# Performance work log

Hardware: AMD Instinct MI355X
Metric: run time of the kernel (lower is better)

Reference implementation:

```python
import jax, jax.numpy as jnp
import numpy as np

B, S, H, NH = 2, 2048, 1024, 16
HD = H // NH  # head_dim = 64
ROPE_BASE = 10000.0


def _rope(x):
    # x: [B, NH, S, HD]; LLaMA-style half-split rotary embedding
    s, d = x.shape[2], x.shape[3]
    inv_freq = 1.0 / (ROPE_BASE ** (jnp.arange(0, d, 2, dtype=jnp.float32) / d))  # [d/2]
    ang = jnp.arange(s, dtype=jnp.float32)[:, None] * inv_freq[None, :]            # [S, d/2]
    cos, sin = jnp.cos(ang), jnp.sin(ang)
    x1, x2 = x[..., : d // 2], x[..., d // 2:]
    return jnp.concatenate([x1 * cos - x2 * sin, x1 * sin + x2 * cos], axis=-1)


def setup_inputs() -> dict:
    key = jax.random.key(0)
    ks = jax.random.split(key, 9)
    hidden_states = jax.random.normal(ks[0], (B, S, H), dtype=jnp.float32)
    # causal mask: True = attend
    causal = jnp.tril(jnp.ones((S, S), dtype=bool))
    attention_mask = jnp.broadcast_to(causal[None, None, :, :], (B, 1, S, S))
    std = 0.02
    wq = jax.random.normal(ks[1], (H, NH * HD), dtype=jnp.float32) * std
    wk = jax.random.normal(ks[2], (H, NH * HD), dtype=jnp.float32) * std
    wv = jax.random.normal(ks[3], (H, NH * HD), dtype=jnp.float32) * std
    wo = jax.random.normal(ks[4], (NH * HD, H), dtype=jnp.float32) * std
    bq = jnp.zeros((NH * HD,), dtype=jnp.float32)
    bk = jnp.zeros((NH * HD,), dtype=jnp.float32)
    bv = jnp.zeros((NH * HD,), dtype=jnp.float32)
    bo = jnp.zeros((H,), dtype=jnp.float32)
    return {"hidden_states": hidden_states, "attention_mask": attention_mask,
            "wq": wq, "bq": bq, "wk": wk, "bk": bk, "wv": wv, "bv": bv,
            "wo": wo, "bo": bo}


def _split_heads(x):
    b, s, _ = x.shape
    return jnp.transpose(x.reshape(b, s, NH, HD), (0, 2, 1, 3))


def reference(hidden_states, attention_mask, wq, bq, wk, bk, wv, bv, wo, bo):
    q = _split_heads(hidden_states @ wq + bq)  # [B,NH,S,HD]
    k = _split_heads(hidden_states @ wk + bk)
    v = _split_heads(hidden_states @ wv + bv)
    q = _rope(q)
    k = _rope(k)
    scores = jnp.einsum('bhqd,bhkd->bhqk', q, k) / jnp.sqrt(jnp.float32(HD))
    scores = jnp.where(attention_mask, scores, jnp.float32(-1e9))
    weights = jax.nn.softmax(scores, axis=-1)
    attn = jnp.einsum('bhqk,bhkv->bhqv', weights, v)  # [B,NH,S,HD]
    attn = jnp.transpose(attn, (0, 2, 1, 3)).reshape(hidden_states.shape[0], attn.shape[2], H)
    return attn @ wo + bo
```

## Files before the change

### kernel.cpp

```cpp
#include <hip/hip_runtime.h>
#include <math.h>

typedef short bf16x8 __attribute__((ext_vector_type(8)));
typedef float f32x4  __attribute__((ext_vector_type(4)));

__device__ __forceinline__ unsigned short f2bf(float f) {
    union { float f; unsigned u; } v; v.f = f;
    unsigned r = v.u + 0x7FFFu + ((v.u >> 16) & 1u);
    return (unsigned short)(r >> 16);
}

#define GLDS16(gp, lp) __builtin_amdgcn_global_load_lds( \
    (const __attribute__((address_space(1))) void*)(gp), \
    (__attribute__((address_space(3))) void*)(lp), 16, 0, 0)


__global__ __launch_bounds__(256)
void prep(const float* __restrict__ X, unsigned short* __restrict__ Xb,
          const float* __restrict__ w0, const float* __restrict__ w1,
          const float* __restrict__ w2, const float* __restrict__ w3,
          unsigned short* o0, unsigned short* o1,
          unsigned short* o2, unsigned short* o3)
{
    const int z = blockIdx.z;
    if (z >= 4) {
        const int lb = (z - 4) * 256 + blockIdx.y * 16 + blockIdx.x;
        const size_t t = (size_t)lb * 256 + threadIdx.x;
        const float4 a = *(const float4*)(X + t * 8);
        const float4 b = *(const float4*)(X + t * 8 + 4);
        unsigned short u[8] = { f2bf(a.x), f2bf(a.y), f2bf(a.z), f2bf(a.w),
                                f2bf(b.x), f2bf(b.y), f2bf(b.z), f2bf(b.w) };
        *(int4*)(Xb + t * 8) = *(int4*)u;
        return;
    }
    const float* W; unsigned short* O;
    switch (z) {
        case 0: W = w0; O = o0; break;
        case 1: W = w1; O = o1; break;
        case 2: W = w2; O = o2; break;
        default: W = w3; O = o3; break;
    }
    __shared__ float T[64][65];
    const int tid = threadIdx.x;
    const int n0 = blockIdx.x * 64, k0 = blockIdx.y * 64;
    #pragma unroll
    for (int i = 0; i < 4; i++) {
        const int k = (tid >> 4) + i * 16, n4 = (tid & 15) * 4;
        const float4 v = *(const float4*)(W + (size_t)(k0 + k) * 1024 + n0 + n4);
        T[k][n4] = v.x; T[k][n4+1] = v.y; T[k][n4+2] = v.z; T[k][n4+3] = v.w;
    }
    __syncthreads();
    if (z == 3) {
        #pragma unroll
        for (int i = 0; i < 4; i++) {
            const int n = (tid >> 4) + i * 16, k4 = (tid & 15) * 4;
            unsigned short u[4];
            #pragma unroll
            for (int j = 0; j < 4; j++) {
                const int q = k4 + j;
                const int p = (q & 3) * 16 + (q >> 2);
                const int d = (p & 3) * 16 + (p >> 2);
                u[j] = f2bf(T[d][n]);
            }
            *(int2*)(O + (size_t)(n0 + n) * 1024 + k0 + k4) = *(int2*)u;
        }
    } else {
        #pragma unroll
        for (int i = 0; i < 4; i++) {
            const int n = (tid >> 4) + i * 16, k4 = (tid & 15) * 4;
            unsigned short u[4] = { f2bf(T[k4][n]), f2bf(T[k4+1][n]),
                                    f2bf(T[k4+2][n]), f2bf(T[k4+3][n]) };
            *(int2*)(O + (size_t)(n0 + n) * 1024 + k0 + k4) = *(int2*)u;
        }
    }
}

__global__ __launch_bounds__(256)
void transpose_v(const unsigned short* __restrict__ Vb, unsigned short* __restrict__ Vtb)
{
    __shared__ unsigned short T[64][72];
    const int tid = threadIdx.x, bh = blockIdx.y, s0 = blockIdx.x * 64;
    const size_t base = (size_t)bh * 2048 * 64;
    #pragma unroll
    for (int i = 0; i < 2; i++) {
        const int s = (tid >> 3) + i * 32, d8 = (tid & 7) * 8;
        *(int4*)&T[s][d8] = *(const int4*)(Vb + base + (size_t)(s0 + s) * 64 + d8);
    }
    __syncthreads();
    #pragma unroll
    for (int i = 0; i < 2; i++) {
        const int d = (tid >> 3) + i * 32, s8 = (tid & 7) * 8;
        unsigned short u[8];
        #pragma unroll
        for (int j = 0; j < 8; j++) u[j] = T[s8 + j][d];
        *(int4*)(Vtb + base + (size_t)d * 2048 + s0 + s8) = *(int4*)u;
    }
}

__global__ __launch_bounds__(256)
void qkv_gemm(const unsigned short* __restrict__ Xb,
              const unsigned short* __restrict__ Wtq, const unsigned short* __restrict__ Wtk,
              const unsigned short* __restrict__ Wtv,
              const float* __restrict__ bq, const float* __restrict__ bk,
              const float* __restrict__ bv,
              unsigned short* __restrict__ Qb, unsigned short* __restrict__ Kb,
              unsigned short* __restrict__ Vb)
{
    const unsigned short* Wt; const float* bias; unsigned short* Out;
    const int z = blockIdx.z;
    if (z == 0)      { Wt = Wtq; bias = bq; Out = Qb; }
    else if (z == 1) { Wt = Wtk; bias = bk; Out = Kb; }
    else             { Wt = Wtv; bias = bv; Out = Vb; }

    __shared__ unsigned short As[128 * 32];
    __shared__ unsigned short Bs[128 * 32];
    const int tid = threadIdx.x, lane = tid & 63, w = tid >> 6;
    const int quad = lane >> 4, c = lane & 15;
    const int wr = w >> 1, wc = w & 1;
    const int m0 = blockIdx.x * 128, n0 = blockIdx.y * 128;
    const int srow = lane >> 2, scol = (lane & 3) * 8;

    f32x4 acc[4][4];
    #pragma unroll
    for (int i = 0; i < 4; i++)
        #pragma unroll
        for (int j = 0; j < 4; j++) acc[i][j] = (f32x4){0.f, 0.f, 0.f, 0.f};

    for (int k0 = 0; k0 < 1024; k0 += 32) {
        #pragma unroll
        for (int j = 0; j < 2; j++) {
            const int r = w * 32 + j * 16;
            GLDS16(Xb + (size_t)(m0 + r + srow) * 1024 + k0 + scol, &As[r * 32]);
            GLDS16(Wt + (size_t)(n0 + r + srow) * 1024 + k0 + scol, &Bs[r * 32]);
        }
        __syncthreads();
        bf16x8 af[4], bf[4];
        #pragma unroll
        for (int rt = 0; rt < 4; rt++)
            af[rt] = *(const bf16x8*)&As[(wr * 64 + rt * 16 + c) * 32 + quad * 8];
        #pragma unroll
        for (int nt = 0; nt < 4; nt++)
            bf[nt] = *(const bf16x8*)&Bs[(wc * 64 + nt * 16 + c) * 32 + quad * 8];
        #pragma unroll
        for (int rt = 0; rt < 4; rt++)
            #pragma unroll
            for (int nt = 0; nt < 4; nt++)
                acc[rt][nt] = __builtin_amdgcn_mfma_f32_16x16x32_bf16(af[rt], bf[nt], acc[rt][nt], 0, 0, 0);
        __syncthreads();
    }

    const int h = (n0 + wc * 64) >> 6;
    const bool rope = (z < 2);
    const float kLn = 9.210340371976184f / 32.0f;
    const float TWO_PI_INV = 0.15915494309189535f;
    const float rv0 = expf(-(float)c * kLn) * TWO_PI_INV;
    const float rv1 = expf(-(float)(c + 16) * kLn) * TWO_PI_INV;
    float bv4[4];
    #pragma unroll
    for (int nt = 0; nt < 4; nt++) bv4[nt] = bias[n0 + wc * 64 + nt * 16 + c];

    #pragma unroll
    for (int rt = 0; rt < 4; rt++) {
        #pragma unroll
        for (int reg = 0; reg < 4; reg++) {
            const int m = m0 + wr * 64 + rt * 16 + quad * 4 + reg;
            const int b = m >> 11, s = m & 2047;
            float x0 = acc[rt][0][reg] + bv4[0];
            float x1 = acc[rt][1][reg] + bv4[1];
            float x2 = acc[rt][2][reg] + bv4[2];
            float x3 = acc[rt][3][reg] + bv4[3];
            float y0 = x0, y1 = x1, y2 = x2, y3 = x3;
            if (rope) {
                float r0 = (float)s * rv0;  r0 -= floorf(r0);
                float r1 = (float)s * rv1;  r1 -= floorf(r1);
                const float sn0 = __builtin_amdgcn_sinf(r0);
                const float cs0 = __builtin_amdgcn_cosf(r0);
                const float sn1 = __builtin_amdgcn_sinf(r1);
                const float cs1 = __builtin_amdgcn_cosf(r1);
                y0 = x0 * cs0 - x2 * sn0;  y2 = x0 * sn0 + x2 * cs0;
                y1 = x1 * cs1 - x3 * sn1;  y3 = x1 * sn1 + x3 * cs1;
            }
            unsigned short u[4] = { f2bf(y0), f2bf(y1), f2bf(y2), f2bf(y3) };
            unsigned short* dst = Out + ((size_t)(b * 16 + h) * 2048 + s) * 64;
            *(int2*)(dst + c * 4) = *(int2*)u;
        }
    }
}

__global__ __launch_bounds__(256)
void out_gemm(const unsigned short* __restrict__ Ab, const unsigned short* __restrict__ Wto,
              const float* __restrict__ bo, float* __restrict__ Out)
{
    __shared__ unsigned short As[128 * 32];
    __shared__ unsigned short Bs[128 * 32];
    const int tid = threadIdx.x, lane = tid & 63, w = tid >> 6;
    const int quad = lane >> 4, c = lane & 15;
    const int wr = w >> 1, wc = w & 1;
    const int m0 = blockIdx.x * 128, n0 = blockIdx.y * 128;
    const int srow = lane >> 2, scol = (lane & 3) * 8;

    f32x4 acc[4][4];
    #pragma unroll
    for (int i = 0; i < 4; i++)
        #pragma unroll
        for (int j = 0; j < 4; j++) acc[i][j] = (f32x4){0.f, 0.f, 0.f, 0.f};

    for (int k0 = 0; k0 < 1024; k0 += 32) {
        #pragma unroll
        for (int j = 0; j < 2; j++) {
            const int r = w * 32 + j * 16;
            GLDS16(Ab  + (size_t)(m0 + r + srow) * 1024 + k0 + scol, &As[r * 32]);
            GLDS16(Wto + (size_t)(n0 + r + srow) * 1024 + k0 + scol, &Bs[r * 32]);
        }
        __syncthreads();
        bf16x8 af[4], bf[4];
        #pragma unroll
        for (int rt = 0; rt < 4; rt++)
            af[rt] = *(const bf16x8*)&As[(wr * 64 + rt * 16 + c) * 32 + quad * 8];
        #pragma unroll
        for (int nt = 0; nt < 4; nt++)
            bf[nt] = *(const bf16x8*)&Bs[(wc * 64 + nt * 16 + c) * 32 + quad * 8];
        #pragma unroll
        for (int rt = 0; rt < 4; rt++)
            #pragma unroll
            for (int nt = 0; nt < 4; nt++)
                acc[rt][nt] = __builtin_amdgcn_mfma_f32_16x16x32_bf16(af[rt], bf[nt], acc[rt][nt], 0, 0, 0);
        __syncthreads();
    }
    #pragma unroll
    for (int rt = 0; rt < 4; rt++) {
        #pragma unroll
        for (int reg = 0; reg < 4; reg++) {
            const int m = m0 + wr * 64 + rt * 16 + quad * 4 + reg;
            #pragma unroll
            for (int nt = 0; nt < 4; nt++) {
                const int n = n0 + wc * 64 + nt * 16 + c;
                Out[(size_t)m * 1024 + n] = acc[rt][nt][reg] + bo[n];
            }
        }
    }
}

__global__ __launch_bounds__(256)
void attn_part(const unsigned short* __restrict__ Qb, const unsigned short* __restrict__ Kb,
               const unsigned short* __restrict__ Vtb, unsigned short* __restrict__ Ab,
               float* __restrict__ Opart, float* __restrict__ Lpart)
{
    __shared__ unsigned short Ks[64 * 72];
    __shared__ unsigned short Vs[65 * 72];
    __shared__ unsigned short Ps[4 * 16 * 72];

    const int tid = threadIdx.x, w = tid >> 6, lane = tid & 63;
    const int quad = lane >> 4, c = lane & 15;
    const int bh = blockIdx.y;
    const int x = (blockIdx.x < 32) ? (int)blockIdx.x + 16 : (int)blockIdx.x - 32;
    int i, start, len;
    if (x < 32) { i = x + 1;  start = 0;  len = (i < 16) ? i : 16; }
    else        { i = x - 15; start = 16; len = i - 16; }
    const int q0 = (i - 1) * 64;
    const bool complete = (start == 0) && (len == i);
    const size_t base = (size_t)bh * 2048 * 64;

    if (tid < 64) Vs[64 * 72 + tid] = 0x3F80;

    const int qbase = q0 + w * 16;
    const int qrow  = qbase + c;
    const size_t qoff = base + (size_t)qrow * 64;
    const bf16x8 qf0 = *(const bf16x8*)(Qb + qoff + quad * 8);
    const bf16x8 qf1 = *(const bf16x8*)(Qb + qoff + 32 + quad * 8);

    f32x4 O[4], Osum;
    Osum = (f32x4){0.f, 0.f, 0.f, 0.f};
    #pragma unroll
    for (int nt = 0; nt < 4; nt++) O[nt] = (f32x4){0.f, 0.f, 0.f, 0.f};

    const int r0s = tid >> 3, r1s = r0s + 32, c8 = (tid & 7) * 8;

    int k0 = start * 64;
    int4 kreg0 = *(const int4*)(Kb  + base + (size_t)(k0 + r0s) * 64 + c8);
    int4 kreg1 = *(const int4*)(Kb  + base + (size_t)(k0 + r1s) * 64 + c8);
    int4 vreg0 = *(const int4*)(Vtb + base + (size_t)r0s * 2048 + k0 + c8);
    int4 vreg1 = *(const int4*)(Vtb + base + (size_t)r1s * 2048 + k0 + c8);

    unsigned short* Pw = Ps + w * 16 * 72;

    for (int t = 0; t < len; t++, k0 += 64) {
        *(int4*)&Ks[(size_t)r0s * 72 + c8] = kreg0;
        *(int4*)&Ks[(size_t)r1s * 72 + c8] = kreg1;
        *(int4*)&Vs[(size_t)r0s * 72 + c8] = vreg0;
        *(int4*)&Vs[(size_t)r1s * 72 + c8] = vreg1;
        __syncthreads();

        if (t + 1 < len) {
            const int kn = k0 + 64;
            kreg0 = *(const int4*)(Kb  + base + (size_t)(kn + r0s) * 64 + c8);
            kreg1 = *(const int4*)(Kb  + base + (size_t)(kn + r1s) * 64 + c8);
            vreg0 = *(const int4*)(Vtb + base + (size_t)r0s * 2048 + kn + c8);
            vreg1 = *(const int4*)(Vtb + base + (size_t)r1s * 2048 + kn + c8);
        }

        const bool need_mask = (k0 + 63) > qbase;

        #pragma unroll
        for (int nt = 0; nt < 4; nt++) {
            const bf16x8 kf0 = *(const bf16x8*)&Ks[(nt * 16 + c) * 72 + quad * 8];
            const bf16x8 kf1 = *(const bf16x8*)&Ks[(nt * 16 + c) * 72 + 32 + quad * 8];
            f32x4 s4 = (f32x4){0.f, 0.f, 0.f, 0.f};
            s4 = __builtin_amdgcn_mfma_f32_16x16x32_bf16(kf0, qf0, s4, 0, 0, 0);
            s4 = __builtin_amdgcn_mfma_f32_16x16x32_bf16(kf1, qf1, s4, 0, 0, 0);
            const int keyb = k0 + nt * 16 + quad * 4;
            unsigned short u[4];
            #pragma unroll
            for (int reg = 0; reg < 4; reg++) {
                float p = __expf(s4[reg] * 0.125f);
                if (need_mask && (keyb + reg > qrow)) p = 0.f;
                u[reg] = f2bf(p);
            }
            *(int2*)&Pw[c * 72 + nt * 16 + quad * 4] = *(int2*)u;
        }

        const bf16x8 pa0 = *(const bf16x8*)&Pw[c * 72 + quad * 8];
        const bf16x8 pa1 = *(const bf16x8*)&Pw[c * 72 + 32 + quad * 8];
        #pragma unroll
        for (int nt = 0; nt < 4; nt++) {
            const bf16x8 vb0 = *(const bf16x8*)&Vs[(nt * 16 + c) * 72 + quad * 8];
            const bf16x8 vb1 = *(const bf16x8*)&Vs[(nt * 16 + c) * 72 + 32 + quad * 8];
            O[nt] = __builtin_amdgcn_mfma_f32_16x16x32_bf16(pa0, vb0, O[nt], 0, 0, 0);
            O[nt] = __builtin_amdgcn_mfma_f32_16x16x32_bf16(pa1, vb1, O[nt], 0, 0, 0);
        }
        const bf16x8 on0 = *(const bf16x8*)&Vs[64 * 72 + quad * 8];
        const bf16x8 on1 = *(const bf16x8*)&Vs[64 * 72 + 32 + quad * 8];
        Osum = __builtin_amdgcn_mfma_f32_16x16x32_bf16(pa0, on0, Osum, 0, 0, 0);
        Osum = __builtin_amdgcn_mfma_f32_16x16x32_bf16(pa1, on1, Osum, 0, 0, 0);
        __syncthreads();
    }

    if (complete) {
        const int b = bh >> 4, h = bh & 15;
        #pragma unroll
        for (int reg = 0; reg < 4; reg++) {
            const float inv = 1.0f / Osum[reg];
            const int q = qbase + quad * 4 + reg;
            unsigned short u[4];
            #pragma unroll
            for (int nt = 0; nt < 4; nt++) u[nt] = f2bf(O[nt][reg] * inv);
            unsigned short* dst = Ab + ((size_t)(b * 2048 + q)) * 1024 + h * 64;
            *(int2*)(dst + c * 4) = *(int2*)u;
        }
    } else {
        const int pslot = (i - 17) * 2 + (start ? 1 : 0);
        float* Op = Opart + ((size_t)bh * 32 + pslot) * 4096;
        float* Lp = Lpart + ((size_t)bh * 32 + pslot) * 64;
        #pragma unroll
        for (int reg = 0; reg < 4; reg++) {
            const int row = w * 16 + quad * 4 + reg;
            float4 o4 = make_float4(O[0][reg], O[1][reg], O[2][reg], O[3][reg]);
            *(float4*)(Op + (size_t)row * 64 + c * 4) = o4;
            if (c == 0) Lp[row] = Osum[reg];
        }
    }
}

__global__ __launch_bounds__(256)
void attn_combine(const float* __restrict__ Opart, const float* __restrict__ Lpart,
                  unsigned short* __restrict__ Ab)
{
    const int tid = threadIdx.x;
    const int j = blockIdx.x, bh = blockIdx.y;
    const int q0 = (j + 16) * 64;
    const size_t s0 = ((size_t)bh * 32 + j * 2) * 4096;
    const size_t l0 = ((size_t)bh * 32 + j * 2) * 64;

    __shared__ float linv[64];
    if (tid < 64) linv[tid] = 1.0f / (Lpart[l0 + tid] + Lpart[l0 + 64 + tid]);
    __syncthreads();

    const int row = tid >> 2, col0 = (tid & 3) * 16;
    const float inv = linv[row];
    const int b = bh >> 4, h = bh & 15;
    const int q = q0 + row;
    unsigned short* dst = Ab + ((size_t)(b * 2048 + q)) * 1024 + h * 64 + col0;
    #pragma unroll
    for (int c4 = 0; c4 < 16; c4 += 4) {
        const float4 a  = *(const float4*)(Opart + s0 + (size_t)row * 64 + col0 + c4);
        const float4 bb = *(const float4*)(Opart + s0 + 4096 + (size_t)row * 64 + col0 + c4);
        dst[c4 + 0] = f2bf((a.x + bb.x) * inv);
        dst[c4 + 1] = f2bf((a.y + bb.y) * inv);
        dst[c4 + 2] = f2bf((a.z + bb.z) * inv);
        dst[c4 + 3] = f2bf((a.w + bb.w) * inv);
    }
}

extern "C" void kernel_launch(void* const* d_in, const int* in_sizes, int n_in,
                              void* d_out, int out_size, void* d_ws, size_t ws_size,
                              hipStream_t stream)
{
    const float* X  = (const float*)d_in[0];
    const float* wq = (const float*)d_in[2];
    const float* bq = (const float*)d_in[3];
    const float* wk = (const float*)d_in[4];
    const float* bk = (const float*)d_in[5];
    const float* wv = (const float*)d_in[6];
    const float* bv = (const float*)d_in[7];
    const float* wo = (const float*)d_in[8];
    const float* bo = (const float*)d_in[9];

    unsigned short* ws = (unsigned short*)d_ws;
    const size_t M1 = 1024 * 1024;
    unsigned short* Xb  = ws;
    unsigned short* Wtq = Xb  + 4 * M1;
    unsigned short* Wtk = Wtq + M1;
    unsigned short* Wtv = Wtk + M1;
    unsigned short* Wto = Wtv + M1;
    unsigned short* Qb  = Wto + M1;
    unsigned short* Kb  = Qb  + 4 * M1;
    unsigned short* Vb  = Kb  + 4 * M1;
    unsigned short* Vtb = Vb  + 4 * M1;
    unsigned short* Ab  = Vtb + 4 * M1;
    float* Opart = (float*)(Ab + 4 * M1);
    float* Lpart = Opart + (size_t)32 * 32 * 4096;

    prep        <<<dim3(16, 16, 12), 256, 0, stream>>>(X, Xb, wq, wk, wv, wo,
                                                       Wtq, Wtk, Wtv, Wto);
    qkv_gemm    <<<dim3(32, 8, 3), 256, 0, stream>>>(Xb, Wtq, Wtk, Wtv, bq, bk, bv, Qb, Kb, Vb);
    transpose_v <<<dim3(32, 32), 256, 0, stream>>>(Vb, Vtb);
    attn_part   <<<dim3(48, 32), 256, 0, stream>>>(Qb, Kb, Vtb, Ab, Opart, Lpart);
    attn_combine<<<dim3(16, 32), 256, 0, stream>>>(Opart, Lpart, Ab);
    out_gemm    <<<dim3(32, 8), 256, 0, stream>>>(Ab, Wto, bo, (float*)d_out);
}
```

Before: 228.5 us.

## Fuse V transpose into QKV GEMM epilogue and double GEMM K-step

The V projection now writes its output directly in the transposed [bh, d, s] layout from the QKV GEMM epilogue, which removes the separate transpose_v kernel launch and one read-write pass over V. Both GEMMs also process 64 K-elements per iteration using two LDS sub-tiles, which halves the number of barrier pairs per tile. The cost is doubled shared memory per block, which may reduce occupancy, and the transposed V stores are narrow 8-byte writes strided by 2048 elements.

```diff
diff --git a/kernel.cpp b/kernel.cpp
--- a/kernel.cpp
+++ b/kernel.cpp
@@ -76,44 +76,22 @@
 }
 
 __global__ __launch_bounds__(256)
-void transpose_v(const unsigned short* __restrict__ Vb, unsigned short* __restrict__ Vtb)
-{
-    __shared__ unsigned short T[64][72];
-    const int tid = threadIdx.x, bh = blockIdx.y, s0 = blockIdx.x * 64;
-    const size_t base = (size_t)bh * 2048 * 64;
-    #pragma unroll
-    for (int i = 0; i < 2; i++) {
-        const int s = (tid >> 3) + i * 32, d8 = (tid & 7) * 8;
-        *(int4*)&T[s][d8] = *(const int4*)(Vb + base + (size_t)(s0 + s) * 64 + d8);
-    }
-    __syncthreads();
-    #pragma unroll
-    for (int i = 0; i < 2; i++) {
-        const int d = (tid >> 3) + i * 32, s8 = (tid & 7) * 8;
-        unsigned short u[8];
-        #pragma unroll
-        for (int j = 0; j < 8; j++) u[j] = T[s8 + j][d];
-        *(int4*)(Vtb + base + (size_t)d * 2048 + s0 + s8) = *(int4*)u;
-    }
-}
-
-__global__ __launch_bounds__(256)
 void qkv_gemm(const unsigned short* __restrict__ Xb,
               const unsigned short* __restrict__ Wtq, const unsigned short* __restrict__ Wtk,
               const unsigned short* __restrict__ Wtv,
               const float* __restrict__ bq, const float* __restrict__ bk,
               const float* __restrict__ bv,
               unsigned short* __restrict__ Qb, unsigned short* __restrict__ Kb,
-              unsigned short* __restrict__ Vb)
+              unsigned short* __restrict__ Vtb)
 {
     const unsigned short* Wt; const float* bias; unsigned short* Out;
     const int z = blockIdx.z;
     if (z == 0)      { Wt = Wtq; bias = bq; Out = Qb; }
     else if (z == 1) { Wt = Wtk; bias = bk; Out = Kb; }
-    else             { Wt = Wtv; bias = bv; Out = Vb; }
-
-    __shared__ unsigned short As[128 * 32];
-    __shared__ unsigned short Bs[128 * 32];
+    else             { Wt = Wtv; bias = bv; Out = Vtb; }
+
+    __shared__ unsigned short As0[128 * 32], As1[128 * 32];
+    __shared__ unsigned short Bs0[128 * 32], Bs1[128 * 32];
     const int tid = threadIdx.x, lane = tid & 63, w = tid >> 6;
     const int quad = lane >> 4, c = lane & 15;
     const int wr = w >> 1, wc = w & 1;
@@ -126,38 +104,67 @@
         #pragma unroll
         for (int j = 0; j < 4; j++) acc[i][j] = (f32x4){0.f, 0.f, 0.f, 0.f};
 
-    for (int k0 = 0; k0 < 1024; k0 += 32) {
+    for (int k0 = 0; k0 < 1024; k0 += 64) {
         #pragma unroll
         for (int j = 0; j < 2; j++) {
             const int r = w * 32 + j * 16;
-            GLDS16(Xb + (size_t)(m0 + r + srow) * 1024 + k0 + scol, &As[r * 32]);
-            GLDS16(Wt + (size_t)(n0 + r + srow) * 1024 + k0 + scol, &Bs[r * 32]);
-        }
-        __syncthreads();
-        bf16x8 af[4], bf[4];
+            const size_t ga = (size_t)(m0 + r + srow) * 1024 + k0 + scol;
+            const size_t gb = (size_t)(n0 + r + srow) * 1024 + k0 + scol;
+            GLDS16(Xb + ga,      &As0[r * 32]);
+            GLDS16(Xb + ga + 32, &As1[r * 32]);
+            GLDS16(Wt + gb,      &Bs0[r * 32]);
+            GLDS16(Wt + gb + 32, &Bs1[r * 32]);
+        }
+        __syncthreads();
+        bf16x8 af0[4], af1[4], bf0[4], bf1[4];
+        #pragma unroll
+        for (int rt = 0; rt < 4; rt++) {
+            const int ro = (wr * 64 + rt * 16 + c) * 32 + quad * 8;
+            af0[rt] = *(const bf16x8*)&As0[ro];
+            af1[rt] = *(const bf16x8*)&As1[ro];
+        }
+        #pragma unroll
+        for (int nt = 0; nt < 4; nt++) {
+            const int ro = (wc * 64 + nt * 16 + c) * 32 + quad * 8;
+            bf0[nt] = *(const bf16x8*)&Bs0[ro];
+            bf1[nt] = *(const bf16x8*)&Bs1[ro];
+        }
         #pragma unroll
         for (int rt = 0; rt < 4; rt++)
-            af[rt] = *(const bf16x8*)&As[(wr * 64 + rt * 16 + c) * 32 + quad * 8];
-        #pragma unroll
-        for (int nt = 0; nt < 4; nt++)
-            bf[nt] = *(const bf16x8*)&Bs[(wc * 64 + nt * 16 + c) * 32 + quad * 8];
-        #pragma unroll
-        for (int rt = 0; rt < 4; rt++)
-            #pragma unroll
-            for (int nt = 0; nt < 4; nt++)
-                acc[rt][nt] = __builtin_amdgcn_mfma_f32_16x16x32_bf16(af[rt], bf[nt], acc[rt][nt], 0, 0, 0);
+            #pragma unroll
+            for (int nt = 0; nt < 4; nt++) {
+                acc[rt][nt] = __builtin_amdgcn_mfma_f32_16x16x32_bf16(af0[rt], bf0[nt], acc[rt][nt], 0, 0, 0);
+                acc[rt][nt] = __builtin_amdgcn_mfma_f32_16x16x32_bf16(af1[rt], bf1[nt], acc[rt][nt], 0, 0, 0);
+            }
         __syncthreads();
     }
 
     const int h = (n0 + wc * 64) >> 6;
-    const bool rope = (z < 2);
+    float bv4[4];
+    #pragma unroll
+    for (int nt = 0; nt < 4; nt++) bv4[nt] = bias[n0 + wc * 64 + nt * 16 + c];
+
+    if (z == 2) {
+        #pragma unroll
+        for (int rt = 0; rt < 4; rt++) {
+            const int s0g = m0 + wr * 64 + rt * 16 + quad * 4;
+            const int b = s0g >> 11, s = s0g & 2047;
+            unsigned short* dstb = Out + (size_t)(b * 16 + h) * 64 * 2048;
+            #pragma unroll
+            for (int nt = 0; nt < 4; nt++) {
+                unsigned short u[4];
+                #pragma unroll
+                for (int reg = 0; reg < 4; reg++) u[reg] = f2bf(acc[rt][nt][reg] + bv4[nt]);
+                *(int2*)(dstb + (size_t)(c * 4 + nt) * 2048 + s) = *(int2*)u;
+            }
+        }
+        return;
+    }
+
     const float kLn = 9.210340371976184f / 32.0f;
     const float TWO_PI_INV = 0.15915494309189535f;
     const float rv0 = expf(-(float)c * kLn) * TWO_PI_INV;
     const float rv1 = expf(-(float)(c + 16) * kLn) * TWO_PI_INV;
-    float bv4[4];
-    #pragma unroll
-    for (int nt = 0; nt < 4; nt++) bv4[nt] = bias[n0 + wc * 64 + nt * 16 + c];
 
     #pragma unroll
     for (int rt = 0; rt < 4; rt++) {
@@ -169,17 +176,14 @@
             float x1 = acc[rt][1][reg] + bv4[1];
             float x2 = acc[rt][2][reg] + bv4[2];
             float x3 = acc[rt][3][reg] + bv4[3];
-            float y0 = x0, y1 = x1, y2 = x2, y3 = x3;
-            if (rope) {
-                float r0 = (float)s * rv0;  r0 -= floorf(r0);
-                float r1 = (float)s * rv1;  r1 -= floorf(r1);
-                const float sn0 = __builtin_amdgcn_sinf(r0);
-                const float cs0 = __builtin_amdgcn_cosf(r0);
-                const float sn1 = __builtin_amdgcn_sinf(r1);
-                const float cs1 = __builtin_amdgcn_cosf(r1);
-                y0 = x0 * cs0 - x2 * sn0;  y2 = x0 * sn0 + x2 * cs0;
-                y1 = x1 * cs1 - x3 * sn1;  y3 = x1 * sn1 + x3 * cs1;
-            }
+            float r0 = (float)s * rv0;  r0 -= floorf(r0);
+            float r1 = (float)s * rv1;  r1 -= floorf(r1);
+            const float sn0 = __builtin_amdgcn_sinf(r0);
+            const float cs0 = __builtin_amdgcn_cosf(r0);
+            const float sn1 = __builtin_amdgcn_sinf(r1);
+            const float cs1 = __builtin_amdgcn_cosf(r1);
+            const float y0 = x0 * cs0 - x2 * sn0, y2 = x0 * sn0 + x2 * cs0;
+            const float y1 = x1 * cs1 - x3 * sn1, y3 = x1 * sn1 + x3 * cs1;
             unsigned short u[4] = { f2bf(y0), f2bf(y1), f2bf(y2), f2bf(y3) };
             unsigned short* dst = Out + ((size_t)(b * 16 + h) * 2048 + s) * 64;
             *(int2*)(dst + c * 4) = *(int2*)u;
@@ -191,8 +195,8 @@
 void out_gemm(const unsigned short* __restrict__ Ab, const unsigned short* __restrict__ Wto,
               const float* __restrict__ bo, float* __restrict__ Out)
 {
-    __shared__ unsigned short As[128 * 32];
-    __shared__ unsigned short Bs[128 * 32];
+    __shared__ unsigned short As0[128 * 32], As1[128 * 32];
+    __shared__ unsigned short Bs0[128 * 32], Bs1[128 * 32];
     const int tid = threadIdx.x, lane = tid & 63, w = tid >> 6;
     const int quad = lane >> 4, c = lane & 15;
     const int wr = w >> 1, wc = w & 1;
@@ -205,26 +209,38 @@
         #pragma unroll
         for (int j = 0; j < 4; j++) acc[i][j] = (f32x4){0.f, 0.f, 0.f, 0.f};
 
-    for (int k0 = 0; k0 < 1024; k0 += 32) {
+    for (int k0 = 0; k0 < 1024; k0 += 64) {
         #pragma unroll
         for (int j = 0; j < 2; j++) {
             const int r = w * 32 + j * 16;
-            GLDS16(Ab  + (size_t)(m0 + r + srow) * 1024 + k0 + scol, &As[r * 32]);
-            GLDS16(Wto + (size_t)(n0 + r + srow) * 1024 + k0 + scol, &Bs[r * 32]);
-        }
-        __syncthreads();
-        bf16x8 af[4], bf[4];
+            const size_t ga = (size_t)(m0 + r + srow) * 1024 + k0 + scol;
+            const size_t gb = (size_t)(n0 + r + srow) * 1024 + k0 + scol;
+            GLDS16(Ab  + ga,      &As0[r * 32]);
+            GLDS16(Ab  + ga + 32, &As1[r * 32]);
+            GLDS16(Wto + gb,      &Bs0[r * 32]);
+            GLDS16(Wto + gb + 32, &Bs1[r * 32]);
+        }
+        __syncthreads();
+        bf16x8 af0[4], af1[4], bf0[4], bf1[4];
+        #pragma unroll
+        for (int rt = 0; rt < 4; rt++) {
+            const int ro = (wr * 64 + rt * 16 + c) * 32 + quad * 8;
+            af0[rt] = *(const bf16x8*)&As0[ro];
+            af1[rt] = *(const bf16x8*)&As1[ro];
+        }
+        #pragma unroll
+        for (int nt = 0; nt < 4; nt++) {
+            const int ro = (wc * 64 + nt * 16 + c) * 32 + quad * 8;
+            bf0[nt] = *(const bf16x8*)&Bs0[ro];
+            bf1[nt] = *(const bf16x8*)&Bs1[ro];
+        }
         #pragma unroll
         for (int rt = 0; rt < 4; rt++)
-            af[rt] = *(const bf16x8*)&As[(wr * 64 + rt * 16 + c) * 32 + quad * 8];
-        #pragma unroll
-        for (int nt = 0; nt < 4; nt++)
-            bf[nt] = *(const bf16x8*)&Bs[(wc * 64 + nt * 16 + c) * 32 + quad * 8];
-        #pragma unroll
-        for (int rt = 0; rt < 4; rt++)
-            #pragma unroll
-            for (int nt = 0; nt < 4; nt++)
-                acc[rt][nt] = __builtin_amdgcn_mfma_f32_16x16x32_bf16(af[rt], bf[nt], acc[rt][nt], 0, 0, 0);
+            #pragma unroll
+            for (int nt = 0; nt < 4; nt++) {
+                acc[rt][nt] = __builtin_amdgcn_mfma_f32_16x16x32_bf16(af0[rt], bf0[nt], acc[rt][nt], 0, 0, 0);
+                acc[rt][nt] = __builtin_amdgcn_mfma_f32_16x16x32_bf16(af1[rt], bf1[nt], acc[rt][nt], 0, 0, 0);
+            }
         __syncthreads();
     }
     #pragma unroll
@@ -414,16 +430,15 @@
     unsigned short* Wto = Wtv + M1;
     unsigned short* Qb  = Wto + M1;
     unsigned short* Kb  = Qb  + 4 * M1;
-    unsigned short* Vb  = Kb  + 4 * M1;
-    unsigned short* Vtb = Vb  + 4 * M1;
+    unsigned short* Vtb = Kb  + 4 * M1;
     unsigned short* Ab  = Vtb + 4 * M1;
     float* Opart = (float*)(Ab + 4 * M1);
     float* Lpart = Opart + (size_t)32 * 32 * 4096;
 
     prep        <<<dim3(16, 16, 12), 256, 0, stream>>>(X, Xb, wq, wk, wv, wo,
                                                        Wtq, Wtk, Wtv, Wto);
-    qkv_gemm    <<<dim3(32, 8, 3), 256, 0, stream>>>(Xb, Wtq, Wtk, Wtv, bq, bk, bv, Qb, Kb, Vb);
-    transpose_v <<<dim3(32, 32), 256, 0, stream>>>(Vb, Vtb);
+    qkv_gemm    <<<dim3(32, 8, 3), 256, 0, stream>>>(Xb, Wtq, Wtk, Wtv, bq, bk, bv,
+                                                     Qb, Kb, Vtb);
     attn_part   <<<dim3(48, 32), 256, 0, stream>>>(Qb, Kb, Vtb, Ab, Opart, Lpart);
     attn_combine<<<dim3(16, 32), 256, 0, stream>>>(Opart, Lpart, Ab);
     out_gemm    <<<dim3(32, 8), 256, 0, stream>>>(Ab, Wto, bo, (float*)d_out);
```

Result: no change. 231.0 us (+1.1%).

## Fuse V transpose into QKV GEMM epilogue and fold softmax scale into Q

Applied to the files above, without the earlier changes.

The V projection blocks now stage their bias-added bf16 tile in shared memory and write V directly in transposed [d][s] layout, which removes the separate transpose_v kernel launch and its extra global read and write of V. The 1/sqrt(d) scale is folded into Q during the RoPE epilogue, dropping a multiply per score in the attention kernel. The ones-row fragment for the row-sum MFMA is loaded once before the key loop instead of on every iteration. In exchange, the GEMM shared buffer grows and the V epilogue adds extra barriers and strided shared-memory reads.

```diff
diff --git a/kernel.cpp b/kernel.cpp
--- a/kernel.cpp
+++ b/kernel.cpp
@@ -76,44 +76,25 @@
 }
 
 __global__ __launch_bounds__(256)
-void transpose_v(const unsigned short* __restrict__ Vb, unsigned short* __restrict__ Vtb)
-{
-    __shared__ unsigned short T[64][72];
-    const int tid = threadIdx.x, bh = blockIdx.y, s0 = blockIdx.x * 64;
-    const size_t base = (size_t)bh * 2048 * 64;
-    #pragma unroll
-    for (int i = 0; i < 2; i++) {
-        const int s = (tid >> 3) + i * 32, d8 = (tid & 7) * 8;
-        *(int4*)&T[s][d8] = *(const int4*)(Vb + base + (size_t)(s0 + s) * 64 + d8);
-    }
-    __syncthreads();
-    #pragma unroll
-    for (int i = 0; i < 2; i++) {
-        const int d = (tid >> 3) + i * 32, s8 = (tid & 7) * 8;
-        unsigned short u[8];
-        #pragma unroll
-        for (int j = 0; j < 8; j++) u[j] = T[s8 + j][d];
-        *(int4*)(Vtb + base + (size_t)d * 2048 + s0 + s8) = *(int4*)u;
-    }
-}
-
-__global__ __launch_bounds__(256)
 void qkv_gemm(const unsigned short* __restrict__ Xb,
               const unsigned short* __restrict__ Wtq, const unsigned short* __restrict__ Wtk,
               const unsigned short* __restrict__ Wtv,
               const float* __restrict__ bq, const float* __restrict__ bk,
               const float* __restrict__ bv,
               unsigned short* __restrict__ Qb, unsigned short* __restrict__ Kb,
-              unsigned short* __restrict__ Vb)
+              unsigned short* __restrict__ Vtb)
 {
     const unsigned short* Wt; const float* bias; unsigned short* Out;
     const int z = blockIdx.z;
     if (z == 0)      { Wt = Wtq; bias = bq; Out = Qb; }
     else if (z == 1) { Wt = Wtk; bias = bk; Out = Kb; }
-    else             { Wt = Wtv; bias = bv; Out = Vb; }
-
-    __shared__ unsigned short As[128 * 32];
-    __shared__ unsigned short Bs[128 * 32];
+    else             { Wt = Wtv; bias = bv; Out = Vtb; }
+
+    __shared__ unsigned short Sh[128 * 72];
+    unsigned short* As = Sh;
+    unsigned short* Bs = Sh + 128 * 32;
+    unsigned short* T  = Sh;
+
     const int tid = threadIdx.x, lane = tid & 63, w = tid >> 6;
     const int quad = lane >> 4, c = lane & 15;
     const int wr = w >> 1, wc = w & 1;
@@ -149,15 +130,48 @@
         __syncthreads();
     }
 
-    const int h = (n0 + wc * 64) >> 6;
-    const bool rope = (z < 2);
+    float bv4[4];
+    #pragma unroll
+    for (int nt = 0; nt < 4; nt++) bv4[nt] = bias[n0 + wc * 64 + nt * 16 + c];
+
+    if (z == 2) {
+        const int b = m0 >> 11, sb = m0 & 2047;
+        const int hgbase = n0 >> 6;
+        #pragma unroll
+        for (int h = 0; h < 2; h++) {
+            if (wc == h) {
+                #pragma unroll
+                for (int rt = 0; rt < 4; rt++)
+                    #pragma unroll
+                    for (int reg = 0; reg < 4; reg++) {
+                        const int s = wr * 64 + rt * 16 + quad * 4 + reg;
+                        unsigned short u[4];
+                        #pragma unroll
+                        for (int nt = 0; nt < 4; nt++)
+                            u[nt] = f2bf(acc[rt][nt][reg] + bv4[nt]);
+                        *(int2*)&T[s * 72 + c * 4] = *(int2*)u;
+                    }
+            }
+            __syncthreads();
+            const int p = tid >> 2, s8 = (tid & 3) * 32;
+            unsigned short* dstb = Vtb + ((size_t)(b * 16 + hgbase + h) * 64 + p) * 2048 + sb;
+            #pragma unroll
+            for (int jj = 0; jj < 32; jj += 8) {
+                unsigned short u[8];
+                #pragma unroll
+                for (int j = 0; j < 8; j++) u[j] = T[(s8 + jj + j) * 72 + p];
+                *(int4*)(dstb + s8 + jj) = *(int4*)u;
+            }
+            __syncthreads();
+        }
+        return;
+    }
+
     const float kLn = 9.210340371976184f / 32.0f;
     const float TWO_PI_INV = 0.15915494309189535f;
     const float rv0 = expf(-(float)c * kLn) * TWO_PI_INV;
     const float rv1 = expf(-(float)(c + 16) * kLn) * TWO_PI_INV;
-    float bv4[4];
-    #pragma unroll
-    for (int nt = 0; nt < 4; nt++) bv4[nt] = bias[n0 + wc * 64 + nt * 16 + c];
+    const float qscale = (z == 0) ? 0.125f : 1.0f;
 
     #pragma unroll
     for (int rt = 0; rt < 4; rt++) {
@@ -169,17 +183,17 @@
             float x1 = acc[rt][1][reg] + bv4[1];
             float x2 = acc[rt][2][reg] + bv4[2];
             float x3 = acc[rt][3][reg] + bv4[3];
-            float y0 = x0, y1 = x1, y2 = x2, y3 = x3;
-            if (rope) {
-                float r0 = (float)s * rv0;  r0 -= floorf(r0);
-                float r1 = (float)s * rv1;  r1 -= floorf(r1);
-                const float sn0 = __builtin_amdgcn_sinf(r0);
-                const float cs0 = __builtin_amdgcn_cosf(r0);
-                const float sn1 = __builtin_amdgcn_sinf(r1);
-                const float cs1 = __builtin_amdgcn_cosf(r1);
-                y0 = x0 * cs0 - x2 * sn0;  y2 = x0 * sn0 + x2 * cs0;
-                y1 = x1 * cs1 - x3 * sn1;  y3 = x1 * sn1 + x3 * cs1;
-            }
+            float r0 = (float)s * rv0;  r0 -= floorf(r0);
+            float r1 = (float)s * rv1;  r1 -= floorf(r1);
+            const float sn0 = __builtin_amdgcn_sinf(r0);
+            const float cs0 = __builtin_amdgcn_cosf(r0);
+            const float sn1 = __builtin_amdgcn_sinf(r1);
+            const float cs1 = __builtin_amdgcn_cosf(r1);
+            const float y0 = (x0 * cs0 - x2 * sn0) * qscale;
+            const float y2 = (x0 * sn0 + x2 * cs0) * qscale;
+            const float y1 = (x1 * cs1 - x3 * sn1) * qscale;
+            const float y3 = (x1 * sn1 + x3 * cs1) * qscale;
+            const int h = (n0 + wc * 64) >> 6;
             unsigned short u[4] = { f2bf(y0), f2bf(y1), f2bf(y2), f2bf(y3) };
             unsigned short* dst = Out + ((size_t)(b * 16 + h) * 2048 + s) * 64;
             *(int2*)(dst + c * 4) = *(int2*)u;
@@ -262,6 +276,9 @@
     const size_t base = (size_t)bh * 2048 * 64;
 
     if (tid < 64) Vs[64 * 72 + tid] = 0x3F80;
+    __syncthreads();
+    const bf16x8 on0 = *(const bf16x8*)&Vs[64 * 72 + quad * 8];
+    const bf16x8 on1 = *(const bf16x8*)&Vs[64 * 72 + 32 + quad * 8];
 
     const int qbase = q0 + w * 16;
     const int qrow  = qbase + c;
@@ -312,7 +329,7 @@
             unsigned short u[4];
             #pragma unroll
             for (int reg = 0; reg < 4; reg++) {
-                float p = __expf(s4[reg] * 0.125f);
+                float p = __expf(s4[reg]);
                 if (need_mask && (keyb + reg > qrow)) p = 0.f;
                 u[reg] = f2bf(p);
             }
@@ -328,8 +345,6 @@
             O[nt] = __builtin_amdgcn_mfma_f32_16x16x32_bf16(pa0, vb0, O[nt], 0, 0, 0);
             O[nt] = __builtin_amdgcn_mfma_f32_16x16x32_bf16(pa1, vb1, O[nt], 0, 0, 0);
         }
-        const bf16x8 on0 = *(const bf16x8*)&Vs[64 * 72 + quad * 8];
-        const bf16x8 on1 = *(const bf16x8*)&Vs[64 * 72 + 32 + quad * 8];
         Osum = __builtin_amdgcn_mfma_f32_16x16x32_bf16(pa0, on0, Osum, 0, 0, 0);
         Osum = __builtin_amdgcn_mfma_f32_16x16x32_bf16(pa1, on1, Osum, 0, 0, 0);
         __syncthreads();
@@ -414,16 +429,15 @@
     unsigned short* Wto = Wtv + M1;
     unsigned short* Qb  = Wto + M1;
     unsigned short* Kb  = Qb  + 4 * M1;
-    unsigned short* Vb  = Kb  + 4 * M1;
-    unsigned short* Vtb = Vb  + 4 * M1;
+    unsigned short* Vtb = Kb  + 4 * M1;
     unsigned short* Ab  = Vtb + 4 * M1;
     float* Opart = (float*)(Ab + 4 * M1);
     float* Lpart = Opart + (size_t)32 * 32 * 4096;
 
     prep        <<<dim3(16, 16, 12), 256, 0, stream>>>(X, Xb, wq, wk, wv, wo,
                                                        Wtq, Wtk, Wtv, Wto);
-    qkv_gemm    <<<dim3(32, 8, 3), 256, 0, stream>>>(Xb, Wtq, Wtk, Wtv, bq, bk, bv, Qb, Kb, Vb);
-    transpose_v <<<dim3(32, 32), 256, 0, stream>>>(Vb, Vtb);
+    qkv_gemm    <<<dim3(32, 8, 3), 256, 0, stream>>>(Xb, Wtq, Wtk, Wtv, bq, bk, bv,
+                                                     Qb, Kb, Vtb);
     attn_part   <<<dim3(48, 32), 256, 0, stream>>>(Qb, Kb, Vtb, Ab, Opart, Lpart);
     attn_combine<<<dim3(16, 32), 256, 0, stream>>>(Opart, Lpart, Ab);
     out_gemm    <<<dim3(32, 8), 256, 0, stream>>>(Ab, Wto, bo, (float*)d_out);
```

Measured after the change: 226.1 us. No clear change (-1.0%).
